# Optimization experiments

Hardware: AMD Instinct MI355X
Metric: run time of the kernel (lower is better)

The kernel has to match this reference:

```python
import jax, jax.numpy as jnp
import numpy as np

# Module hyperparameters (from init_kwargs)
HID = 2048          # hidden_dim
LAT = 512           # kv_latent_dim
H = 16              # num_heads
D = HID // H        # head_dim = 128
FORGET_P = 0.1      # forget_prob
WIN = 128           # window_size
SINK = 16           # persistent_tokens
B, S = 2, 2048
NEG = -1e9


def setup_inputs() -> dict:
    key = jax.random.key(0)
    ks = jax.random.split(key, 8)
    scale = 0.02
    x = jax.random.normal(ks[0], (B, S, HID), dtype=jnp.float32)
    W_q = jax.random.normal(ks[1], (HID, HID), dtype=jnp.float32) * scale
    W_dkv = jax.random.normal(ks[2], (HID, LAT), dtype=jnp.float32) * scale
    W_uk = jax.random.normal(ks[3], (LAT, HID), dtype=jnp.float32) * scale
    W_uv = jax.random.normal(ks[4], (LAT, HID), dtype=jnp.float32) * scale
    W_o = jax.random.normal(ks[5], (HID, HID), dtype=jnp.float32) * scale
    # Bernoulli(forget_prob) per-key forget mask (1 = forget this token)
    forget_mask = jax.random.bernoulli(ks[6], FORGET_P, (B, S)).astype(jnp.int32)
    return {"x": x, "W_q": W_q, "W_dkv": W_dkv, "W_uk": W_uk,
            "W_uv": W_uv, "W_o": W_o, "forget_mask": forget_mask, "top_k": 64}


def reference(x, W_q, W_dkv, W_uk, W_uv, W_o, forget_mask, top_k):
    Bx, Sx, _ = x.shape
    # Queries; keys/values via shared compressed KV latent (MLA-style)
    q = (x @ W_q).reshape(Bx, Sx, H, D)
    c = x @ W_dkv                                   # [B, S, LAT]
    k = (c @ W_uk).reshape(Bx, Sx, H, D)
    v = (c @ W_uv).reshape(Bx, Sx, H, D)

    scores = jnp.einsum('bqhd,bkhd->bhqk', q, k) / np.float32(np.sqrt(D))

    qi = jnp.arange(Sx)[:, None]
    ki = jnp.arange(Sx)[None, :]
    causal = ki <= qi
    local = ki >= qi - (WIN - 1)
    sink = ki < SINK                  # persistent sink tokens always visible
    allow = causal & (local | sink)   # [S, S]

    # Forgetting: drop non-sink, non-self keys flagged by the forget mask
    forget = (forget_mask[:, None, None, :] == 1) \
             & (ki >= SINK)[None, None] & (ki != qi)[None, None]   # [B,1,S,S]
    keep = allow[None, None] & ~forget

    s = jnp.where(keep, scores, jnp.asarray(NEG, scores.dtype))
    # Top-k selection per query: keep only the k largest scores
    kth = jax.lax.top_k(s, top_k)[0][..., -1:]
    s = jnp.where(s >= kth, s, jnp.asarray(NEG, s.dtype))

    attn = jax.nn.softmax(s, axis=-1)
    out = jnp.einsum('bhqk,bkhd->bqhd', attn, v).reshape(Bx, Sx, HID)
    return out @ W_o
```

## Files before the change

### kernel.cpp

```cpp
#include <hip/hip_runtime.h>
#include <hip/hip_bf16.h>

typedef unsigned short u16;
typedef unsigned int u32;
typedef unsigned long long u64;
typedef __bf16 bf16x8 __attribute__((ext_vector_type(8)));
typedef float f32x4 __attribute__((ext_vector_type(4)));
typedef u16 u16x4 __attribute__((ext_vector_type(4)));
typedef u16 u16x8 __attribute__((ext_vector_type(8)));

static constexpr int BB = 2, SS = 2048, HIDC = 2048, LATC = 512, NH = 16, HD = 128;
static constexpr int MROWS = BB * SS;
static constexpr float NEGV = -1e9f;

__device__ __forceinline__ u16 f2bf(float f) {
  __hip_bfloat16 h = __float2bfloat16(f);
  return __builtin_bit_cast(u16, h);
}
__device__ __forceinline__ float bf2f(u16 u) {
  return __uint_as_float(((u32)u) << 16);
}
__device__ __forceinline__ void load_lds16(const void* g, void* l) {
  __builtin_amdgcn_global_load_lds(
      (const __attribute__((address_space(1))) void*)g,
      (__attribute__((address_space(3))) void*)l, 16, 0, 0);
}

template <int MODE>
__global__ __launch_bounds__(256, 2) void gemm_bt(
    const u16* __restrict__ A, const u16* __restrict__ Bt,
    float* __restrict__ C, u16* __restrict__ Cb, int M, int N, int K,
    size_t sA, size_t sB, size_t sC) {
  __shared__ u16 As[128 * 64];
  __shared__ u16 Bs[128 * 64];
  const int tid = threadIdx.x;
  const int lane = tid & 63;
  const int wv = tid >> 6;
  const int wr = wv >> 1, wc = wv & 1;
  const int m0 = blockIdx.x * 128, n0 = blockIdx.y * 128;
  A += sA * blockIdx.z;
  Bt += sB * blockIdx.z;
  if constexpr (MODE == 0) C += sC * blockIdx.z;
  if constexpr (MODE == 2) Cb += sC * blockIdx.z;

  f32x4 acc[4][4];
#pragma unroll
  for (int i = 0; i < 4; ++i)
#pragma unroll
    for (int j = 0; j < 4; ++j) acc[i][j] = (f32x4){0.f, 0.f, 0.f, 0.f};

  int srow[4], sgc[4];
#pragma unroll
  for (int j = 0; j < 4; ++j) {
    int e = j * 2048 + tid * 8;
    int row = e >> 6;
    int slot = (e >> 3) & 7;
    srow[j] = row;
    sgc[j] = (slot ^ (row & 7)) * 8;
  }

  for (int k0 = 0; k0 < K; k0 += 64) {
    __syncthreads();
#pragma unroll
    for (int j = 0; j < 4; ++j) {
      const u16* ga = A + (size_t)(m0 + srow[j]) * K + k0 + sgc[j];
      const u16* gb = Bt + (size_t)(n0 + srow[j]) * K + k0 + sgc[j];
      load_lds16(ga, &As[j * 2048 + wv * 512]);
      load_lds16(gb, &Bs[j * 2048 + wv * 512]);
    }
    asm volatile("s_waitcnt vmcnt(0)" ::: "memory");
    __syncthreads();

#pragma unroll
    for (int kk = 0; kk < 2; ++kk) {
      bf16x8 afr[4], bfr[4];
      const int kg = kk * 4 + (lane >> 4);
#pragma unroll
      for (int i = 0; i < 4; ++i) {
        int ar = wr * 64 + i * 16 + (lane & 15);
        afr[i] = *(const bf16x8*)&As[ar * 64 + ((kg ^ (ar & 7)) << 3)];
        int br = wc * 64 + i * 16 + (lane & 15);
        bfr[i] = *(const bf16x8*)&Bs[br * 64 + ((kg ^ (br & 7)) << 3)];
      }
#pragma unroll
      for (int mi = 0; mi < 4; ++mi)
#pragma unroll
        for (int ni = 0; ni < 4; ++ni)
          acc[mi][ni] = __builtin_amdgcn_mfma_f32_16x16x32_bf16(
              afr[mi], bfr[ni], acc[mi][ni], 0, 0, 0);
    }
  }

#pragma unroll
  for (int mi = 0; mi < 4; ++mi) {
#pragma unroll
    for (int ni = 0; ni < 4; ++ni) {
      const int row = m0 + wr * 64 + mi * 16 + (lane >> 4) * 4;
      const int col = n0 + wc * 64 + ni * 16 + (lane & 15);
#pragma unroll
      for (int r = 0; r < 4; ++r) {
        size_t off = (size_t)(row + r) * N + col;
        if constexpr (MODE == 0) C[off] = acc[mi][ni][r];
        if constexpr (MODE == 2) Cb[off] = f2bf(acc[mi][ni][r]);
      }
    }
  }
}

template <int TN, int MODE>
__global__ __launch_bounds__(256, 2) void gemm_split_bt(
    const u16* __restrict__ Ah, const u16* __restrict__ Al,
    const u16* __restrict__ Bth, const u16* __restrict__ Btl,
    float* __restrict__ C, u16* __restrict__ Ch, u16* __restrict__ Cl,
    int M, int N, int K) {
  constexpr int NI = TN / 32;
  __shared__ u16 Ash[128 * 64];
  __shared__ u16 Asl[128 * 64];
  __shared__ u16 Bsh[TN * 64];
  __shared__ u16 Bsl[TN * 64];
  const int tid = threadIdx.x;
  const int lane = tid & 63;
  const int wv = tid >> 6;
  const int wr = wv >> 1, wc = wv & 1;
  const int l15 = lane & 15, lhi = lane >> 4;
  const int m0 = blockIdx.x * 128, n0 = blockIdx.y * TN;

  f32x4 acc[4][NI];
#pragma unroll
  for (int i = 0; i < 4; ++i)
#pragma unroll
    for (int j = 0; j < NI; ++j) acc[i][j] = (f32x4){0.f, 0.f, 0.f, 0.f};

  int srow[4], sgc[4];
#pragma unroll
  for (int j = 0; j < 4; ++j) {
    int e = j * 2048 + tid * 8;
    int row = e >> 6;
    int slot = (e >> 3) & 7;
    srow[j] = row;
    sgc[j] = (slot ^ (row & 7)) * 8;
  }

  for (int k0 = 0; k0 < K; k0 += 64) {
    __syncthreads();
#pragma unroll
    for (int j = 0; j < 4; ++j) {
      const size_t ao = (size_t)(m0 + srow[j]) * K + k0 + sgc[j];
      load_lds16(Ah + ao, &Ash[j * 2048 + wv * 512]);
      load_lds16(Al + ao, &Asl[j * 2048 + wv * 512]);
    }
#pragma unroll
    for (int j = 0; j < NI; ++j) {
      const size_t bo = (size_t)(n0 + srow[j]) * K + k0 + sgc[j];
      load_lds16(Bth + bo, &Bsh[j * 2048 + wv * 512]);
      load_lds16(Btl + bo, &Bsl[j * 2048 + wv * 512]);
    }
    asm volatile("s_waitcnt vmcnt(0)" ::: "memory");
    __syncthreads();

#pragma unroll
    for (int kk = 0; kk < 2; ++kk) {
      const int kg = kk * 4 + lhi;
      bf16x8 afh[4], afl[4], bfh[NI], bfl[NI];
#pragma unroll
      for (int i = 0; i < 4; ++i) {
        const int ar = wr * 64 + i * 16 + l15;
        const int off = ar * 64 + ((kg ^ (ar & 7)) << 3);
        afh[i] = *(const bf16x8*)&Ash[off];
        afl[i] = *(const bf16x8*)&Asl[off];
      }
#pragma unroll
      for (int i = 0; i < NI; ++i) {
        const int br = wc * (TN / 2) + i * 16 + l15;
        const int off = br * 64 + ((kg ^ (br & 7)) << 3);
        bfh[i] = *(const bf16x8*)&Bsh[off];
        bfl[i] = *(const bf16x8*)&Bsl[off];
      }
#pragma unroll
      for (int mi = 0; mi < 4; ++mi)
#pragma unroll
        for (int ni = 0; ni < NI; ++ni) {
          acc[mi][ni] = __builtin_amdgcn_mfma_f32_16x16x32_bf16(
              afh[mi], bfh[ni], acc[mi][ni], 0, 0, 0);
          acc[mi][ni] = __builtin_amdgcn_mfma_f32_16x16x32_bf16(
              afh[mi], bfl[ni], acc[mi][ni], 0, 0, 0);
          acc[mi][ni] = __builtin_amdgcn_mfma_f32_16x16x32_bf16(
              afl[mi], bfh[ni], acc[mi][ni], 0, 0, 0);
        }
    }
  }

#pragma unroll
  for (int mi = 0; mi < 4; ++mi) {
#pragma unroll
    for (int ni = 0; ni < NI; ++ni) {
      const int row = m0 + wr * 64 + mi * 16 + lhi * 4;
      const int col = n0 + wc * (TN / 2) + ni * 16 + l15;
#pragma unroll
      for (int r = 0; r < 4; ++r) {
        const size_t off = (size_t)(row + r) * N + col;
        const float v = acc[mi][ni][r];
        if constexpr (MODE == 0) C[off] = v;
        if constexpr (MODE == 3) {
          const u16 hh = f2bf(v);
          Ch[off] = hh;
          Cl[off] = f2bf(v - bf2f(hh));
        }
      }
    }
  }
}

__global__ __launch_bounds__(256) void prep_all(
    const float* __restrict__ x, u16* __restrict__ xh, u16* __restrict__ xl,
    const float* __restrict__ Wq, u16* __restrict__ Wqh, u16* __restrict__ Wql,
    const float* __restrict__ Wdkv, u16* __restrict__ Wdh, u16* __restrict__ Wdl,
    const float* __restrict__ Wuk, u16* __restrict__ Wukh, u16* __restrict__ Wukl,
    const float* __restrict__ Wuv, u16* __restrict__ Wuvt,
    const float* __restrict__ Wo, u16* __restrict__ Wot) {
  const int bx = blockIdx.x, tid = threadIdx.x;
  if (bx < 8192) {
    const size_t i = ((size_t)bx * 256 + tid) * 4;
    f32x4 v = *(const f32x4*)(x + i);
    u16x4 hh, ll;
#pragma unroll
    for (int e = 0; e < 4; ++e) {
      const u16 hi = f2bf(v[e]);
      hh[e] = hi;
      ll[e] = f2bf(v[e] - bf2f(hi));
    }
    *(u16x4*)(xh + i) = hh;
    *(u16x4*)(xl + i) = ll;
    return;
  }
  __shared__ float t[32][33];
  const float* W;
  u16 *Th, *Tl = nullptr;
  int K, N, gx, gy;
  if (bx < 12288) {
    const int q = bx - 8192;
    W = Wq; Th = Wqh; Tl = Wql; K = 2048; N = 2048; gx = q & 63; gy = q >> 6;
  } else if (bx < 13312) {
    const int q = bx - 12288;
    W = Wdkv; Th = Wdh; Tl = Wdl; K = 2048; N = 512; gx = q & 15; gy = q >> 4;
  } else if (bx < 14336) {
    const int q = bx - 13312;
    W = Wuk; Th = Wukh; Tl = Wukl; K = 512; N = 2048; gx = q & 63; gy = q >> 6;
  } else if (bx < 15360) {
    const int q = bx - 14336;
    W = Wuv; Th = Wuvt; K = 512; N = 2048; gx = q & 63; gy = q >> 6;
  } else {
    const int q = bx - 15360;
    W = Wo; Th = Wot; K = 2048; N = 2048; gx = q & 63; gy = q >> 6;
  }
  const int tx = tid & 31, ty0 = tid >> 5;
#pragma unroll
  for (int i = 0; i < 4; ++i) {
    const int ty = ty0 + i * 8;
    t[ty][tx] = W[(size_t)(gy * 32 + ty) * N + gx * 32 + tx];
  }
  __syncthreads();
#pragma unroll
  for (int i = 0; i < 4; ++i) {
    const int ty = ty0 + i * 8;
    const float v = t[tx][ty];
    const size_t o = (size_t)(gx * 32 + ty) * K + gy * 32 + tx;
    const u16 hi = f2bf(v);
    Th[o] = hi;
    if (Tl) Tl[o] = f2bf(v - bf2f(hi));
  }
}

__device__ __forceinline__ u32 fmap(float f) {
  u32 b = __float_as_uint(f);
  return (b & 0x80000000u) ? ~b : (b | 0x80000000u);
}
__device__ __forceinline__ float unfmap(u32 u) {
  return (u & 0x80000000u) ? __uint_as_float(u ^ 0x80000000u)
                           : __uint_as_float(~u);
}

__global__ __launch_bounds__(512, 2) void attn_v7(
    const u16* __restrict__ qbh, const u16* __restrict__ qbl,
    const u16* __restrict__ khi, const u16* __restrict__ klo,
    const u16* __restrict__ vt, const int* __restrict__ forget,
    const int* __restrict__ topk, u16* __restrict__ ab) {
  __shared__ u16 KP[2 * 64 * 128];
  __shared__ float St[64 * 68];
  __shared__ u16 Vb1[64 * 128];
  __shared__ int fm[256];
  u16* const Kh = KP;
  u16* const Kl = KP + 64 * 128;
  u16* const Pb = KP;
  u16* const Vt0 = (u16*)St;

  const float scale = 0.08838834764831845f;
  const int tid = threadIdx.x, lane = tid & 63, wv = tid >> 6;
  const int lin = blockIdx.x + 32 * (blockIdx.y + 16 * blockIdx.z);
  const int nl = (lin & 7) * 128 + (lin >> 3);
  const int q0 = (nl & 31) * 64;
  const int h = (nl >> 5) & 15;
  const int b = nl >> 9;
  const int mt = wv >> 1, nh = wv & 1;
  const int l15 = lane & 15, lhi = lane >> 4;
  const int nt = (q0 >= 256) ? 4 : (q0 / 64 + 1);
  const int KTOP = topk[0];

  auto kbase = [&](int t) {
    return (q0 >= 256) ? (t == 0 ? 0 : q0 + t * 64 - 192) : t * 64;
  };
  auto stage_k = [&](int t) {
    const int kbt = kbase(t);
#pragma unroll
    for (int p = 0; p < 2; ++p) {
      const int c = p * 512 + tid;
      const int row = c >> 4, sl = c & 15;
      const size_t src = (size_t)(b * SS + kbt + row) * HIDC + h * HD +
                         ((sl ^ (row & 7)) << 3);
      load_lds16(khi + src, Kh + (p * 512 + wv * 64) * 8);
      load_lds16(klo + src, Kl + (p * 512 + wv * 64) * 8);
    }
  };
  auto stage_vt = [&](int t, u16* dst) {
    const int kbt = kbase(t);
#pragma unroll
    for (int p = 0; p < 2; ++p) {
      const int c = p * 512 + tid;
      const int d = c >> 3, sl = c & 7;
      const u16* src = vt + ((size_t)(b * HIDC + h * HD + d)) * SS + kbt +
                       ((sl ^ (d & 7)) << 3);
      load_lds16(src, dst + (p * 512 + wv * 64) * 8);
    }
  };

  if (tid < 256)
    fm[tid] = ((tid >> 6) < nt) ? forget[b * SS + kbase(tid >> 6) + (tid & 63)] : 0;

  u32 koff[4][2];
#pragma unroll
  for (int kt = 0; kt < 4; ++kt)
#pragma unroll
    for (int ni = 0; ni < 2; ++ni) {
      const int key = nh * 32 + ni * 16 + l15;
      const int kg = kt * 4 + lhi;
      koff[kt][ni] = key * 128 + ((kg ^ (key & 7)) << 3);
    }
  const int arow = mt * 16 + l15;
  u32 pboff[2];
#pragma unroll
  for (int ks = 0; ks < 2; ++ks)
    pboff[ks] = arow * 256 + (((ks * 4 + lhi) ^ (arow & 7)) << 3);
  u32 voff[2][4];
#pragma unroll
  for (int ks = 0; ks < 2; ++ks)
#pragma unroll
    for (int t2 = 0; t2 < 4; ++t2) {
      const int drow = nh * 64 + t2 * 16 + l15;
      voff[ks][t2] = drow * 64 + (((ks * 4 + lhi) ^ (drow & 7)) << 3);
    }
  const u32 stw = (u32)(mt * 16 + lhi * 4) * 68 + nh * 32 + l15;

  u16x8 ah[4], al[4];
  const size_t qrow = (size_t)(b * SS + q0 + mt * 16 + l15) * HIDC + h * HD;
#pragma unroll
  for (int kt = 0; kt < 4; ++kt) {
    ah[kt] = *(const u16x8*)(qbh + qrow + kt * 32 + lhi * 8);
    al[kt] = *(const u16x8*)(qbl + qrow + kt * 32 + lhi * 8);
  }

  u32 uu[8][4];
#pragma unroll
  for (int i = 0; i < 8; ++i)
#pragma unroll
    for (int j = 0; j < 4; ++j) uu[i][j] = 0u;

  stage_k(0);
  stage_vt(0, Vb1);

#pragma unroll
  for (int t = 0; t < 4; ++t) {
    if (t < nt) {
      asm volatile("s_waitcnt vmcnt(0)" ::: "memory");
      __syncthreads();

      f32x4 acc0 = (f32x4){0.f, 0.f, 0.f, 0.f};
      f32x4 acc1 = (f32x4){0.f, 0.f, 0.f, 0.f};
#pragma unroll
      for (int kt = 0; kt < 4; ++kt) {
#pragma unroll
        for (int ni = 0; ni < 2; ++ni) {
          const bf16x8 bh = *(const bf16x8*)(Kh + koff[kt][ni]);
          const bf16x8 bl = *(const bf16x8*)(Kl + koff[kt][ni]);
          f32x4 a = ni ? acc1 : acc0;
          a = __builtin_amdgcn_mfma_f32_16x16x32_bf16(
              __builtin_bit_cast(bf16x8, ah[kt]), bh, a, 0, 0, 0);
          a = __builtin_amdgcn_mfma_f32_16x16x32_bf16(
              __builtin_bit_cast(bf16x8, ah[kt]), bl, a, 0, 0, 0);
          a = __builtin_amdgcn_mfma_f32_16x16x32_bf16(
              __builtin_bit_cast(bf16x8, al[kt]), bh, a, 0, 0, 0);
          if (ni) acc1 = a; else acc0 = a;
        }
      }
#pragma unroll
      for (int ni = 0; ni < 2; ++ni)
#pragma unroll
        for (int r = 0; r < 4; ++r)
          St[stw + r * 68 + ni * 16] = (ni ? acc1 : acc0)[r] * scale;
      __syncthreads();

      if (t + 1 < nt) stage_k(t + 1);

      const int kbt = kbase(t);
      const int key = kbt + lane;
      const bool fok = !(fm[t * 64 + lane] != 0 && key >= 16);
      const bool sk = key < 16;
#pragma unroll
      for (int i = 0; i < 8; ++i) {
        const int qi = q0 + wv * 8 + i;
        const bool valid =
            key <= qi && (key >= qi - 127 || sk) && (fok || key == qi);
        uu[i][t] = fmap(valid ? St[(wv * 8 + i) * 68 + lane] : NEGV);
      }
    }
  }
  __syncthreads();

  if (nt > 1) stage_vt(1, Vt0);

  u32 tl[8], th[8];
#pragma unroll
  for (int i = 0; i < 8; ++i) { tl[i] = 0u; th[i] = 0xFFFFFFFFu; }
  for (int it = 0; it < 32; ++it) {
    bool any = false;
#pragma unroll
    for (int i = 0; i < 8; ++i) {
      if (tl[i] < th[i]) {
        any = true;
        const u32 mid = tl[i] + ((th[i] - tl[i]) >> 1) + 1u;
        const int cnt = __popcll(__ballot(uu[i][0] >= mid)) +
                        __popcll(__ballot(uu[i][1] >= mid)) +
                        __popcll(__ballot(uu[i][2] >= mid)) +
                        __popcll(__ballot(uu[i][3] >= mid));
        if (cnt == KTOP) {
          tl[i] = mid;
          th[i] = mid;
        } else if (cnt > KTOP) {
          tl[i] = mid;
        } else {
          th[i] = mid - 1u;
        }
      }
    }
    if (!any) break;
  }

#pragma unroll
  for (int i = 0; i < 8; ++i) {
    const int r = wv * 8 + i;
    float sv[4], m = NEGV;
#pragma unroll
    for (int j = 0; j < 4; ++j) {
      sv[j] = unfmap(uu[i][j]);
      m = (uu[i][j] >= tl[i]) ? fmaxf(m, sv[j]) : m;
    }
#pragma unroll
    for (int off = 32; off > 0; off >>= 1) m = fmaxf(m, __shfl_xor(m, off));
    float e[4], z = 0.f;
#pragma unroll
    for (int j = 0; j < 4; ++j) {
      e[j] = (uu[i][j] >= tl[i]) ? __expf(sv[j] - m) : 0.f;
      z += e[j];
    }
#pragma unroll
    for (int off = 32; off > 0; off >>= 1) z += __shfl_xor(z, off);
    const float rz = 1.f / z;
#pragma unroll
    for (int j = 0; j < 4; ++j) {
      const int c = lane + 64 * j;
      const int sl = c >> 3;
      Pb[r * 256 + ((sl ^ (r & 7)) << 3) + (c & 7)] = f2bf(e[j] * rz);
    }
  }

  asm volatile("s_waitcnt vmcnt(0)" ::: "memory");
  __syncthreads();

  f32x4 pacc[4];
#pragma unroll
  for (int t2 = 0; t2 < 4; ++t2) pacc[t2] = (f32x4){0.f, 0.f, 0.f, 0.f};

#pragma unroll
  for (int t = 0; t < 4; ++t) {
    if (t < nt) {
      if (t == 2) {
        if (nt > 3) asm volatile("s_waitcnt vmcnt(2)" ::: "memory");
        else asm volatile("s_waitcnt vmcnt(0)" ::: "memory");
        __syncthreads();
      }
      if (t == 3) {
        asm volatile("s_waitcnt vmcnt(0)" ::: "memory");
        __syncthreads();
      }
      u16* const Vcur = (t & 1) ? Vt0 : Vb1;
#pragma unroll
      for (int ks = 0; ks < 2; ++ks) {
        const bf16x8 af = *(const bf16x8*)(Pb + pboff[ks] + t * 64);
#pragma unroll
        for (int t2 = 0; t2 < 4; ++t2) {
          const bf16x8 bf_ = *(const bf16x8*)(Vcur + voff[ks][t2]);
          pacc[t2] = __builtin_amdgcn_mfma_f32_16x16x32_bf16(af, bf_, pacc[t2],
                                                             0, 0, 0);
        }
      }
      if (t + 2 < nt) {
        __syncthreads();
        stage_vt(t + 2, Vcur);
      }
    }
  }

#pragma unroll
  for (int t2 = 0; t2 < 4; ++t2)
#pragma unroll
    for (int r = 0; r < 4; ++r) {
      const int row = q0 + mt * 16 + lhi * 4 + r;
      const int col = h * HD + nh * 64 + t2 * 16 + l15;
      ab[(size_t)(b * SS + row) * HIDC + col] = f2bf(pacc[t2][r]);
    }
}

extern "C" void kernel_launch(void* const* d_in, const int* in_sizes, int n_in,
                              void* d_out, int out_size, void* d_ws, size_t ws_size,
                              hipStream_t stream) {
  const float* x = (const float*)d_in[0];
  const float* W_q = (const float*)d_in[1];
  const float* W_dkv = (const float*)d_in[2];
  const float* W_uk = (const float*)d_in[3];
  const float* W_uv = (const float*)d_in[4];
  const float* W_o = (const float*)d_in[5];
  const int* forget = (const int*)d_in[6];
  const int* topk = (const int*)d_in[7];
  float* out = (float*)d_out;

  char* p = (char*)d_ws;
  auto take = [&](size_t n) {
    char* r = p;
    p += (n + 255) & ~(size_t)255;
    return r;
  };

  u16* xb_hi = (u16*)take((size_t)MROWS * HIDC * 2);
  u16* xb_lo = (u16*)take((size_t)MROWS * HIDC * 2);
  u16* Wqh = (u16*)take((size_t)HIDC * HIDC * 2);
  u16* Wql = (u16*)take((size_t)HIDC * HIDC * 2);
  u16* Wdh = (u16*)take((size_t)LATC * HIDC * 2);
  u16* Wdl = (u16*)take((size_t)LATC * HIDC * 2);
  u16* Wukh = (u16*)take((size_t)HIDC * LATC * 2);
  u16* Wukl = (u16*)take((size_t)HIDC * LATC * 2);
  u16* Wuvt = (u16*)take((size_t)HIDC * LATC * 2);
  u16* Wot = (u16*)take((size_t)HIDC * HIDC * 2);
  u16* qbh = (u16*)take((size_t)MROWS * HIDC * 2);
  u16* qbl = (u16*)take((size_t)MROWS * HIDC * 2);
  u16* cbh = (u16*)take((size_t)MROWS * LATC * 2);
  u16* cbl = (u16*)take((size_t)MROWS * LATC * 2);
  u16* vt = (u16*)take((size_t)BB * HIDC * SS * 2);
  u16* khi = xb_hi;
  u16* klo = xb_lo;
  u16* ab = Wqh;

  prep_all<<<dim3(19456), dim3(256), 0, stream>>>(
      x, xb_hi, xb_lo, W_q, Wqh, Wql, W_dkv, Wdh, Wdl, W_uk, Wukh, Wukl,
      W_uv, Wuvt, W_o, Wot);

  gemm_split_bt<128, 3><<<dim3(MROWS / 128, HIDC / 128), 256, 0, stream>>>(
      xb_hi, xb_lo, Wqh, Wql, nullptr, qbh, qbl, MROWS, HIDC, HIDC);
  gemm_split_bt<64, 3><<<dim3(MROWS / 128, LATC / 64), 256, 0, stream>>>(
      xb_hi, xb_lo, Wdh, Wdl, nullptr, cbh, cbl, MROWS, LATC, HIDC);
  gemm_split_bt<128, 3><<<dim3(MROWS / 128, HIDC / 128), 256, 0, stream>>>(
      cbh, cbl, Wukh, Wukl, nullptr, khi, klo, MROWS, HIDC, LATC);
  gemm_bt<2><<<dim3(HIDC / 128, SS / 128, BB), 256, 0, stream>>>(
      Wuvt, cbh, nullptr, vt, HIDC, SS, LATC,
      0, (size_t)SS * LATC, (size_t)HIDC * SS);
  attn_v7<<<dim3(SS / 64, NH, BB), dim3(512), 0, stream>>>(
      qbh, qbl, khi, klo, vt, forget, topk, ab);
  gemm_bt<0><<<dim3(MROWS / 128, HIDC / 128), 256, 0, stream>>>(
      ab, Wot, out, nullptr, MROWS, HIDC, HIDC, 0, 0, 0);
}
```

Baseline: 308.1 us.

## Merge independent projection GEMMs into two combined launches with interleaved block zones

Result: slower. 318.7 us (+3.4%).

```diff
diff --git a/kernel.cpp b/kernel.cpp
--- a/kernel.cpp
+++ b/kernel.cpp
@@ -26,11 +26,212 @@
       (__attribute__((address_space(3))) void*)l, 16, 0, 0);
 }
 
-template <int MODE>
-__global__ __launch_bounds__(256, 2) void gemm_bt(
+__device__ __forceinline__ void split_body(
+    u16* __restrict__ Ash, u16* __restrict__ Asl,
+    u16* __restrict__ Bsh, u16* __restrict__ Bsl,
+    const u16* __restrict__ Ah, const u16* __restrict__ Al,
+    const u16* __restrict__ Bth, const u16* __restrict__ Btl,
+    u16* __restrict__ Ch, u16* __restrict__ Cl, int N, int K, int m0, int n0) {
+  const int tid = threadIdx.x;
+  const int lane = tid & 63;
+  const int wv = tid >> 6;
+  const int wr = wv >> 1, wc = wv & 1;
+  const int l15 = lane & 15, lhi = lane >> 4;
+
+  f32x4 acc[4][4];
+#pragma unroll
+  for (int i = 0; i < 4; ++i)
+#pragma unroll
+    for (int j = 0; j < 4; ++j) acc[i][j] = (f32x4){0.f, 0.f, 0.f, 0.f};
+
+  int srow[4], sgc[4];
+#pragma unroll
+  for (int j = 0; j < 4; ++j) {
+    int e = j * 2048 + tid * 8;
+    int row = e >> 6;
+    int slot = (e >> 3) & 7;
+    srow[j] = row;
+    sgc[j] = (slot ^ (row & 7)) * 8;
+  }
+
+  for (int k0 = 0; k0 < K; k0 += 64) {
+    __syncthreads();
+#pragma unroll
+    for (int j = 0; j < 4; ++j) {
+      const size_t ao = (size_t)(m0 + srow[j]) * K + k0 + sgc[j];
+      load_lds16(Ah + ao, &Ash[j * 2048 + wv * 512]);
+      load_lds16(Al + ao, &Asl[j * 2048 + wv * 512]);
+      const size_t bo = (size_t)(n0 + srow[j]) * K + k0 + sgc[j];
+      load_lds16(Bth + bo, &Bsh[j * 2048 + wv * 512]);
+      load_lds16(Btl + bo, &Bsl[j * 2048 + wv * 512]);
+    }
+    asm volatile("s_waitcnt vmcnt(0)" ::: "memory");
+    __syncthreads();
+
+#pragma unroll
+    for (int kk = 0; kk < 2; ++kk) {
+      const int kg = kk * 4 + lhi;
+      bf16x8 afh[4], afl[4], bfh[4], bfl[4];
+#pragma unroll
+      for (int i = 0; i < 4; ++i) {
+        const int ar = wr * 64 + i * 16 + l15;
+        const int offa = ar * 64 + ((kg ^ (ar & 7)) << 3);
+        afh[i] = *(const bf16x8*)&Ash[offa];
+        afl[i] = *(const bf16x8*)&Asl[offa];
+        const int br = wc * 64 + i * 16 + l15;
+        const int offb = br * 64 + ((kg ^ (br & 7)) << 3);
+        bfh[i] = *(const bf16x8*)&Bsh[offb];
+        bfl[i] = *(const bf16x8*)&Bsl[offb];
+      }
+#pragma unroll
+      for (int mi = 0; mi < 4; ++mi)
+#pragma unroll
+        for (int ni = 0; ni < 4; ++ni) {
+          acc[mi][ni] = __builtin_amdgcn_mfma_f32_16x16x32_bf16(
+              afh[mi], bfh[ni], acc[mi][ni], 0, 0, 0);
+          acc[mi][ni] = __builtin_amdgcn_mfma_f32_16x16x32_bf16(
+              afh[mi], bfl[ni], acc[mi][ni], 0, 0, 0);
+          acc[mi][ni] = __builtin_amdgcn_mfma_f32_16x16x32_bf16(
+              afl[mi], bfh[ni], acc[mi][ni], 0, 0, 0);
+        }
+    }
+  }
+
+#pragma unroll
+  for (int mi = 0; mi < 4; ++mi) {
+#pragma unroll
+    for (int ni = 0; ni < 4; ++ni) {
+      const int row = m0 + wr * 64 + mi * 16 + lhi * 4;
+      const int col = n0 + wc * 64 + ni * 16 + l15;
+#pragma unroll
+      for (int r = 0; r < 4; ++r) {
+        const size_t off = (size_t)(row + r) * N + col;
+        const float v = acc[mi][ni][r];
+        const u16 hh = f2bf(v);
+        Ch[off] = hh;
+        Cl[off] = f2bf(v - bf2f(hh));
+      }
+    }
+  }
+}
+
+__device__ __forceinline__ void plain_bf16_body(
+    u16* __restrict__ As, u16* __restrict__ Bs, const u16* __restrict__ A,
+    const u16* __restrict__ Bt, u16* __restrict__ Cb, int N, int K, int m0,
+    int n0) {
+  const int tid = threadIdx.x;
+  const int lane = tid & 63;
+  const int wv = tid >> 6;
+  const int wr = wv >> 1, wc = wv & 1;
+
+  f32x4 acc[4][4];
+#pragma unroll
+  for (int i = 0; i < 4; ++i)
+#pragma unroll
+    for (int j = 0; j < 4; ++j) acc[i][j] = (f32x4){0.f, 0.f, 0.f, 0.f};
+
+  int srow[4], sgc[4];
+#pragma unroll
+  for (int j = 0; j < 4; ++j) {
+    int e = j * 2048 + tid * 8;
+    int row = e >> 6;
+    int slot = (e >> 3) & 7;
+    srow[j] = row;
+    sgc[j] = (slot ^ (row & 7)) * 8;
+  }
+
+  for (int k0 = 0; k0 < K; k0 += 64) {
+    __syncthreads();
+#pragma unroll
+    for (int j = 0; j < 4; ++j) {
+      const u16* ga = A + (size_t)(m0 + srow[j]) * K + k0 + sgc[j];
+      const u16* gb = Bt + (size_t)(n0 + srow[j]) * K + k0 + sgc[j];
+      load_lds16(ga, &As[j * 2048 + wv * 512]);
+      load_lds16(gb, &Bs[j * 2048 + wv * 512]);
+    }
+    asm volatile("s_waitcnt vmcnt(0)" ::: "memory");
+    __syncthreads();
+
+#pragma unroll
+    for (int kk = 0; kk < 2; ++kk) {
+      bf16x8 afr[4], bfr[4];
+      const int kg = kk * 4 + (lane >> 4);
+#pragma unroll
+      for (int i = 0; i < 4; ++i) {
+        int ar = wr * 64 + i * 16 + (lane & 15);
+        afr[i] = *(const bf16x8*)&As[ar * 64 + ((kg ^ (ar & 7)) << 3)];
+        int br = wc * 64 + i * 16 + (lane & 15);
+        bfr[i] = *(const bf16x8*)&Bs[br * 64 + ((kg ^ (br & 7)) << 3)];
+      }
+#pragma unroll
+      for (int mi = 0; mi < 4; ++mi)
+#pragma unroll
+        for (int ni = 0; ni < 4; ++ni)
+          acc[mi][ni] = __builtin_amdgcn_mfma_f32_16x16x32_bf16(
+              afr[mi], bfr[ni], acc[mi][ni], 0, 0, 0);
+    }
+  }
+
+#pragma unroll
+  for (int mi = 0; mi < 4; ++mi) {
+#pragma unroll
+    for (int ni = 0; ni < 4; ++ni) {
+      const int row = m0 + wr * 64 + mi * 16 + (lane >> 4) * 4;
+      const int col = n0 + wc * 64 + ni * 16 + (lane & 15);
+#pragma unroll
+      for (int r = 0; r < 4; ++r)
+        Cb[(size_t)(row + r) * N + col] = f2bf(acc[mi][ni][r]);
+    }
+  }
+}
+
+__global__ __launch_bounds__(256, 2) void gemm_qc(
+    const u16* __restrict__ xh, const u16* __restrict__ xl,
+    const u16* __restrict__ Wqh, const u16* __restrict__ Wql,
+    const u16* __restrict__ Wdh, const u16* __restrict__ Wdl,
+    u16* __restrict__ qbh, u16* __restrict__ qbl, u16* __restrict__ cbh,
+    u16* __restrict__ cbl) {
+  __shared__ u16 Ash[128 * 64];
+  __shared__ u16 Asl[128 * 64];
+  __shared__ u16 Bsh[128 * 64];
+  __shared__ u16 Bsl[128 * 64];
+  const int bz = blockIdx.x;
+  int zone, idx;
+  if (bz < 256) { zone = bz & 1; idx = bz >> 1; }
+  else { zone = 0; idx = bz - 128; }
+  if (zone == 0) {
+    split_body(Ash, Asl, Bsh, Bsl, xh, xl, Wqh, Wql, qbh, qbl, HIDC, HIDC,
+               (idx & 31) * 128, (idx >> 5) * 128);
+  } else {
+    split_body(Ash, Asl, Bsh, Bsl, xh, xl, Wdh, Wdl, cbh, cbl, LATC, HIDC,
+               (idx & 31) * 128, (idx >> 5) * 128);
+  }
+}
+
+__global__ __launch_bounds__(256, 2) void gemm_kvt(
+    const u16* __restrict__ cbh, const u16* __restrict__ cbl,
+    const u16* __restrict__ Wukh, const u16* __restrict__ Wukl,
+    u16* __restrict__ khi, u16* __restrict__ klo,
+    const u16* __restrict__ Wuvt, u16* __restrict__ vt) {
+  __shared__ u16 Ash[128 * 64];
+  __shared__ u16 Asl[128 * 64];
+  __shared__ u16 Bsh[128 * 64];
+  __shared__ u16 Bsl[128 * 64];
+  const int bz = blockIdx.x;
+  const int zone = bz & 1, idx = bz >> 1;
+  if (zone == 0) {
+    split_body(Ash, Asl, Bsh, Bsl, cbh, cbl, Wukh, Wukl, khi, klo, HIDC, LATC,
+               (idx & 31) * 128, (idx >> 5) * 128);
+  } else {
+    const int zb = idx >> 8, m = idx & 15, n = (idx >> 4) & 15;
+    plain_bf16_body(Ash, Bsh, Wuvt, cbh + (size_t)SS * LATC * zb,
+                    vt + (size_t)HIDC * SS * zb, SS, LATC, m * 128, n * 128);
+  }
+}
+
+__global__ __launch_bounds__(256, 2) void gemm_out(
     const u16* __restrict__ A, const u16* __restrict__ Bt,
-    float* __restrict__ C, u16* __restrict__ Cb, int M, int N, int K,
-    size_t sA, size_t sB, size_t sC) {
+    float* __restrict__ C, int M, int N, int K) {
   __shared__ u16 As[128 * 64];
   __shared__ u16 Bs[128 * 64];
   const int tid = threadIdx.x;
@@ -38,10 +239,6 @@
   const int wv = tid >> 6;
   const int wr = wv >> 1, wc = wv & 1;
   const int m0 = blockIdx.x * 128, n0 = blockIdx.y * 128;
-  A += sA * blockIdx.z;
-  Bt += sB * blockIdx.z;
-  if constexpr (MODE == 0) C += sC * blockIdx.z;
-  if constexpr (MODE == 2) Cb += sC * blockIdx.z;
 
   f32x4 acc[4][4];
 #pragma unroll
@@ -98,115 +295,8 @@
       const int row = m0 + wr * 64 + mi * 16 + (lane >> 4) * 4;
       const int col = n0 + wc * 64 + ni * 16 + (lane & 15);
 #pragma unroll
-      for (int r = 0; r < 4; ++r) {
-        size_t off = (size_t)(row + r) * N + col;
-        if constexpr (MODE == 0) C[off] = acc[mi][ni][r];
-        if constexpr (MODE == 2) Cb[off] = f2bf(acc[mi][ni][r]);
-      }
-    }
-  }
-}
-
-template <int TN, int MODE>
-__global__ __launch_bounds__(256, 2) void gemm_split_bt(
-    const u16* __restrict__ Ah, const u16* __restrict__ Al,
-    const u16* __restrict__ Bth, const u16* __restrict__ Btl,
-    float* __restrict__ C, u16* __restrict__ Ch, u16* __restrict__ Cl,
-    int M, int N, int K) {
-  constexpr int NI = TN / 32;
-  __shared__ u16 Ash[128 * 64];
-  __shared__ u16 Asl[128 * 64];
-  __shared__ u16 Bsh[TN * 64];
-  __shared__ u16 Bsl[TN * 64];
-  const int tid = threadIdx.x;
-  const int lane = tid & 63;
-  const int wv = tid >> 6;
-  const int wr = wv >> 1, wc = wv & 1;
-  const int l15 = lane & 15, lhi = lane >> 4;
-  const int m0 = blockIdx.x * 128, n0 = blockIdx.y * TN;
-
-  f32x4 acc[4][NI];
-#pragma unroll
-  for (int i = 0; i < 4; ++i)
-#pragma unroll
-    for (int j = 0; j < NI; ++j) acc[i][j] = (f32x4){0.f, 0.f, 0.f, 0.f};
-
-  int srow[4], sgc[4];
-#pragma unroll
-  for (int j = 0; j < 4; ++j) {
-    int e = j * 2048 + tid * 8;
-    int row = e >> 6;
-    int slot = (e >> 3) & 7;
-    srow[j] = row;
-    sgc[j] = (slot ^ (row & 7)) * 8;
-  }
-
-  for (int k0 = 0; k0 < K; k0 += 64) {
-    __syncthreads();
-#pragma unroll
-    for (int j = 0; j < 4; ++j) {
-      const size_t ao = (size_t)(m0 + srow[j]) * K + k0 + sgc[j];
-      load_lds16(Ah + ao, &Ash[j * 2048 + wv * 512]);
-      load_lds16(Al + ao, &Asl[j * 2048 + wv * 512]);
-    }
-#pragma unroll
-    for (int j = 0; j < NI; ++j) {
-      const size_t bo = (size_t)(n0 + srow[j]) * K + k0 + sgc[j];
-      load_lds16(Bth + bo, &Bsh[j * 2048 + wv * 512]);
-      load_lds16(Btl + bo, &Bsl[j * 2048 + wv * 512]);
-    }
-    asm volatile("s_waitcnt vmcnt(0)" ::: "memory");
-    __syncthreads();
-
-#pragma unroll
-    for (int kk = 0; kk < 2; ++kk) {
-      const int kg = kk * 4 + lhi;
-      bf16x8 afh[4], afl[4], bfh[NI], bfl[NI];
-#pragma unroll
-      for (int i = 0; i < 4; ++i) {
-        const int ar = wr * 64 + i * 16 + l15;
-        const int off = ar * 64 + ((kg ^ (ar & 7)) << 3);
-        afh[i] = *(const bf16x8*)&Ash[off];
-        afl[i] = *(const bf16x8*)&Asl[off];
-      }
-#pragma unroll
-      for (int i = 0; i < NI; ++i) {
-        const int br = wc * (TN / 2) + i * 16 + l15;
-        const int off = br * 64 + ((kg ^ (br & 7)) << 3);
-        bfh[i] = *(const bf16x8*)&Bsh[off];
-        bfl[i] = *(const bf16x8*)&Bsl[off];
-      }
-#pragma unroll
-      for (int mi = 0; mi < 4; ++mi)
-#pragma unroll
-        for (int ni = 0; ni < NI; ++ni) {
-          acc[mi][ni] = __builtin_amdgcn_mfma_f32_16x16x32_bf16(
-              afh[mi], bfh[ni], acc[mi][ni], 0, 0, 0);
-          acc[mi][ni] = __builtin_amdgcn_mfma_f32_16x16x32_bf16(
-              afh[mi], bfl[ni], acc[mi][ni], 0, 0, 0);
-          acc[mi][ni] = __builtin_amdgcn_mfma_f32_16x16x32_bf16(
-              afl[mi], bfh[ni], acc[mi][ni], 0, 0, 0);
-        }
-    }
-  }
-
-#pragma unroll
-  for (int mi = 0; mi < 4; ++mi) {
-#pragma unroll
-    for (int ni = 0; ni < NI; ++ni) {
-      const int row = m0 + wr * 64 + mi * 16 + lhi * 4;
-      const int col = n0 + wc * (TN / 2) + ni * 16 + l15;
-#pragma unroll
-      for (int r = 0; r < 4; ++r) {
-        const size_t off = (size_t)(row + r) * N + col;
-        const float v = acc[mi][ni][r];
-        if constexpr (MODE == 0) C[off] = v;
-        if constexpr (MODE == 3) {
-          const u16 hh = f2bf(v);
-          Ch[off] = hh;
-          Cl[off] = f2bf(v - bf2f(hh));
-        }
-      }
+      for (int r = 0; r < 4; ++r)
+        C[(size_t)(row + r) * N + col] = acc[mi][ni][r];
     }
   }
 }
@@ -571,18 +661,12 @@
   prep_all<<<dim3(19456), dim3(256), 0, stream>>>(
       x, xb_hi, xb_lo, W_q, Wqh, Wql, W_dkv, Wdh, Wdl, W_uk, Wukh, Wukl,
       W_uv, Wuvt, W_o, Wot);
-
-  gemm_split_bt<128, 3><<<dim3(MROWS / 128, HIDC / 128), 256, 0, stream>>>(
-      xb_hi, xb_lo, Wqh, Wql, nullptr, qbh, qbl, MROWS, HIDC, HIDC);
-  gemm_split_bt<64, 3><<<dim3(MROWS / 128, LATC / 64), 256, 0, stream>>>(
-      xb_hi, xb_lo, Wdh, Wdl, nullptr, cbh, cbl, MROWS, LATC, HIDC);
-  gemm_split_bt<128, 3><<<dim3(MROWS / 128, HIDC / 128), 256, 0, stream>>>(
-      cbh, cbl, Wukh, Wukl, nullptr, khi, klo, MROWS, HIDC, LATC);
-  gemm_bt<2><<<dim3(HIDC / 128, SS / 128, BB), 256, 0, stream>>>(
-      Wuvt, cbh, nullptr, vt, HIDC, SS, LATC,
-      0, (size_t)SS * LATC, (size_t)HIDC * SS);
+  gemm_qc<<<dim3(640), dim3(256), 0, stream>>>(
+      xb_hi, xb_lo, Wqh, Wql, Wdh, Wdl, qbh, qbl, cbh, cbl);
+  gemm_kvt<<<dim3(1024), dim3(256), 0, stream>>>(
+      cbh, cbl, Wukh, Wukl, khi, klo, Wuvt, vt);
   attn_v7<<<dim3(SS / 64, NH, BB), dim3(512), 0, stream>>>(
       qbh, qbl, khi, klo, vt, forget, topk, ab);
-  gemm_bt<0><<<dim3(MROWS / 128, HIDC / 128), 256, 0, stream>>>(
-      ab, Wot, out, nullptr, MROWS, HIDC, HIDC, 0, 0, 0);
-}
+  gemm_out<<<dim3(MROWS / 128, HIDC / 128), 256, 0, stream>>>(
+      ab, Wot, out, MROWS, HIDC, HIDC);
+}
```
